# Kernel optimization log

Measured on AMD Instinct MI355X. Metric: run time of the kernel, lower is better.

## Reference

```python
import jax, jax.numpy as jnp
import numpy as np

N_NODES = 100000


def setup_inputs() -> dict:
    key = jax.random.key(0)
    ks = jax.random.split(key, 4)
    x = jax.random.normal(ks[0], (N_NODES, 128), dtype=jnp.float32)
    edge_index = jax.random.randint(ks[1], (2, 1600000), 0, N_NODES, dtype=jnp.int64)
    W1 = jax.random.normal(ks[2], (128, 64), dtype=jnp.float32) * (1.0 / np.sqrt(128))
    b1 = jnp.zeros((64,), dtype=jnp.float32)
    W2 = jax.random.normal(ks[3], (64, 64), dtype=jnp.float32) * (1.0 / np.sqrt(64))
    b2 = jnp.zeros((64,), dtype=jnp.float32)
    return {"x": x, "edge_index": edge_index, "W1": W1, "b1": b1, "W2": W2, "b2": b2}


def reference(x, edge_index, W1, b1, W2, b2):
    N = x.shape[0]
    loop = jnp.arange(N, dtype=edge_index.dtype)
    src = jnp.concatenate([edge_index[0], loop])  # [E+N] sources (incl. self-loops)
    dst = jnp.concatenate([edge_index[1], loop])  # [E+N] targets
    # symmetric GCN normalization: deg counts edge weights (all 1) at target nodes
    deg = jax.ops.segment_sum(jnp.ones_like(src, dtype=x.dtype), dst, num_segments=N)
    dinv = jnp.where(deg > 0, jax.lax.rsqrt(deg), 0.0)
    norm = (dinv[src] * dinv[dst])[:, None]  # [E+N, 1]

    def gcn_conv(h, W, b):
        h = h @ W                                   # dense transform [N, out]
        msg = h[src] * norm                         # gather + normalize [E+N, out]
        agg = jax.ops.segment_sum(msg, dst, num_segments=N)  # scatter-add
        return agg + b

    h = jax.nn.gelu(gcn_conv(x, W1, b1), approximate=False)  # torch nn.GELU = exact erf
    return gcn_conv(h, W2, b2)
```

## Files before the change

kernel.cpp:

```cpp
#include <hip/hip_runtime.h>
#include <math.h>

#define N_NODES 100000
#define N_EDGES 1600000
#define NBUK 782
#define BCAP 2600
#define BINCHUNK 4096

typedef unsigned short u16;
typedef u16 u16x4 __attribute__((ext_vector_type(4)));
typedef u16 u16x8 __attribute__((ext_vector_type(8)));
typedef short s16x8 __attribute__((ext_vector_type(8)));
typedef float f32x4 __attribute__((ext_vector_type(4)));

__device__ __forceinline__ float bf2f(u16 u) {
    union { unsigned i; float f; } v; v.i = ((unsigned)u) << 16; return v.f;
}
__device__ __forceinline__ u16 f2bf(float f) {
    union { float f; unsigned i; } v; v.f = f;
    return (u16)((v.i + 0x7FFFu + ((v.i >> 16) & 1u)) >> 16);
}

__global__ __launch_bounds__(256) void k_bin(const int* __restrict__ src,
                                             const int* __restrict__ dst,
                                             int* bucketCursor,
                                             unsigned int* __restrict__ bins) {
    __shared__ int lcnt[NBUK];
    __shared__ int lbase[NBUK];
    const int t = threadIdx.x;
    for (int i = t; i < NBUK; i += 256) lcnt[i] = 0;
    __syncthreads();

    const int e0 = blockIdx.x * BINCHUNK + t * 16;
    int4 s4[4], d4[4];
    int bkt[16], rnk[16];
    const bool valid = e0 < N_EDGES;
    if (valid) {
        #pragma unroll
        for (int k = 0; k < 4; ++k) {
            s4[k] = *(const int4*)(src + e0 + 4 * k);
            d4[k] = *(const int4*)(dst + e0 + 4 * k);
        }
        #pragma unroll
        for (int k = 0; k < 4; ++k) {
            int dd[4] = { d4[k].x, d4[k].y, d4[k].z, d4[k].w };
            #pragma unroll
            for (int j = 0; j < 4; ++j) {
                int b = dd[j] >> 7;
                bkt[4 * k + j] = b;
                rnk[4 * k + j] = atomicAdd(&lcnt[b], 1);
            }
        }
    }
    __syncthreads();
    for (int i = t; i < NBUK; i += 256)
        if (lcnt[i] > 0) lbase[i] = atomicAdd(&bucketCursor[i], lcnt[i]);
    __syncthreads();
    if (valid) {
        #pragma unroll
        for (int k = 0; k < 4; ++k) {
            int ss[4] = { s4[k].x, s4[k].y, s4[k].z, s4[k].w };
            int dd[4] = { d4[k].x, d4[k].y, d4[k].z, d4[k].w };
            #pragma unroll
            for (int j = 0; j < 4; ++j) {
                int i = 4 * k + j;
                unsigned w = ((unsigned)(dd[j] & 127) << 17) | (unsigned)ss[j];
                bins[(size_t)bkt[i] * BCAP + lbase[bkt[i]] + rnk[i]] = w;
            }
        }
    }
}

__global__ __launch_bounds__(256) void k_bscan(const int* __restrict__ bucketCursor,
                                               int* __restrict__ gBase,
                                               int* __restrict__ row_start) {
    __shared__ int sd[256];
    const int t = threadIdx.x;
    const int idx0 = t * 4;
    int v0 = (idx0 + 0 < NBUK) ? bucketCursor[idx0 + 0] : 0;
    int v1 = (idx0 + 1 < NBUK) ? bucketCursor[idx0 + 1] : 0;
    int v2 = (idx0 + 2 < NBUK) ? bucketCursor[idx0 + 2] : 0;
    int v3 = (idx0 + 3 < NBUK) ? bucketCursor[idx0 + 3] : 0;
    int s0 = v0, s1 = s0 + v1, s2 = s1 + v2, s3 = s2 + v3;
    sd[t] = s3;
    __syncthreads();
    #pragma unroll
    for (int off = 1; off < 256; off <<= 1) {
        int x = (t >= off) ? sd[t - off] : 0;
        __syncthreads();
        sd[t] += x;
        __syncthreads();
    }
    int excl = (t > 0) ? sd[t - 1] : 0;
    if (idx0 + 0 < NBUK) gBase[idx0 + 0] = excl;
    if (idx0 + 1 < NBUK) gBase[idx0 + 1] = excl + s0;
    if (idx0 + 2 < NBUK) gBase[idx0 + 2] = excl + s1;
    if (idx0 + 3 < NBUK) gBase[idx0 + 3] = excl + s2;
    if (t == 0) row_start[N_NODES] = N_EDGES;
}

__global__ __launch_bounds__(256) void k_build(const unsigned int* __restrict__ bins,
                                               const int* __restrict__ bucketCursor,
                                               const int* __restrict__ gBase,
                                               int* __restrict__ row_start,
                                               float* __restrict__ dinv,
                                               int* __restrict__ csr_src) {
    __shared__ int cnt[128];
    __shared__ int ps[128];
    __shared__ int cur[128];
    const int b = blockIdx.x;
    const int t = threadIdx.x;
    const int bcnt = bucketCursor[b];
    const int gb = gBase[b];
    const unsigned int* mybins = bins + (size_t)b * BCAP;

    if (t < 128) cnt[t] = 0;
    __syncthreads();
    for (int i = t; i < bcnt; i += 256)
        atomicAdd(&cnt[mybins[i] >> 17], 1);
    __syncthreads();
    if (t < 128) ps[t] = cnt[t];
    __syncthreads();
    #pragma unroll
    for (int off = 1; off < 128; off <<= 1) {
        int x = (t >= off && t < 128) ? ps[t - off] : 0;
        __syncthreads();
        if (t < 128) ps[t] += x;
        __syncthreads();
    }
    if (t < 128) {
        int excl = (t > 0) ? ps[t - 1] : 0;
        cur[t] = excl;
        int node = (b << 7) + t;
        if (node < N_NODES) {
            row_start[node] = gb + excl;
            dinv[node] = rsqrtf((float)(cnt[t] + 1));
        }
    }
    __syncthreads();
    for (int i = t; i < bcnt; i += 256) {
        unsigned w = mybins[i];
        int dl = w >> 17;
        int s = (int)(w & 0x1FFFFu);
        int p = atomicAdd(&cur[dl], 1);
        csr_src[gb + p] = s;
    }
}

__global__ __launch_bounds__(256) void k_wsplit(const float* __restrict__ W1,
                                                const float* __restrict__ W2,
                                                u16* __restrict__ w1pre,
                                                u16* __restrict__ w2pre) {
    const int t = threadIdx.x;
    #pragma unroll
    for (int i = 0; i < 32; ++i) {
        int e = i * 256 + t;
        int k = e >> 6, c = e & 63;
        float f = W1[e];
        u16 h = f2bf(f);
        u16 l = f2bf(f - bf2f(h));
        int byte = (c * 256 + k * 2) ^ ((c & 7) << 4);
        *(u16*)((char*)w1pre + byte) = h;
        *(u16*)((char*)w1pre + 16384 + byte) = l;
    }
    #pragma unroll
    for (int i = 0; i < 16; ++i) {
        int e = i * 256 + t;
        int k = e >> 6, c = e & 63;
        float f = W2[e];
        u16 h = f2bf(f);
        u16 l = f2bf(f - bf2f(h));
        int byte = (c * 128 + k * 2) ^ ((c & 7) << 4);
        *(u16*)((char*)w2pre + byte) = h;
        *(u16*)((char*)w2pre + 8192 + byte) = l;
    }
}

__global__ __launch_bounds__(256) void k_gemm1(const float* __restrict__ X,
                                               const u16* __restrict__ w1pre,
                                               const float* __restrict__ dinv,
                                               u16* __restrict__ H) {
    __shared__ u16 sxh[64 * 128];
    __shared__ u16 sxl[64 * 128];
    __shared__ u16 wth[64 * 128];
    __shared__ u16 wtl[64 * 128];
    const int t = threadIdx.x;
    const int blk = blockIdx.x;

    {
        const float4* Xv = (const float4*)X;
        #pragma unroll
        for (int i = 0; i < 8; ++i) {
            int idx = i * 256 + t;
            int row = idx >> 5;
            int k4  = (idx & 31) << 2;
            int grow = blk * 64 + row;
            float4 v = make_float4(0.f, 0.f, 0.f, 0.f);
            if (grow < N_NODES) v = Xv[(size_t)grow * 32 + (idx & 31)];
            float f[4] = { v.x, v.y, v.z, v.w };
            u16x4 hv, lv;
            #pragma unroll
            for (int j = 0; j < 4; ++j) {
                u16 h = f2bf(f[j]);
                hv[j] = h;
                lv[j] = f2bf(f[j] - bf2f(h));
            }
            int byte = (row * 256 + k4 * 2) ^ ((row & 7) << 4);
            *(u16x4*)((char*)sxh + byte) = hv;
            *(u16x4*)((char*)sxl + byte) = lv;
        }
    }
    {
        const u16x8* G = (const u16x8*)w1pre;
        u16x8* Lh = (u16x8*)wth;
        u16x8* Ll = (u16x8*)wtl;
        #pragma unroll
        for (int i = 0; i < 4; ++i) Lh[i * 256 + t] = G[i * 256 + t];
        #pragma unroll
        for (int i = 0; i < 4; ++i) Ll[i * 256 + t] = G[1024 + i * 256 + t];
    }
    __syncthreads();

    const int lane = t & 63;
    const int w    = t >> 6;
    const int l16  = lane & 15;
    const int kg   = lane >> 4;
    f32x4 acc[4];
    #pragma unroll
    for (int nt = 0; nt < 4; ++nt)
        #pragma unroll
        for (int j = 0; j < 4; ++j) acc[nt][j] = 0.f;

    const int arow = w * 16 + l16;
    const int aswz = (arow & 7) << 4;
    #pragma unroll
    for (int kt = 0; kt < 4; ++kt) {
        const int koff = kt * 64 + kg * 16;
        s16x8 ah = *(const s16x8*)((const char*)sxh + ((arow * 256 + koff) ^ aswz));
        s16x8 al = *(const s16x8*)((const char*)sxl + ((arow * 256 + koff) ^ aswz));
        #pragma unroll
        for (int nt = 0; nt < 4; ++nt) {
            const int c = nt * 16 + l16;
            const int wb = (c * 256 + koff) ^ ((c & 7) << 4);
            s16x8 bh = *(const s16x8*)((const char*)wth + wb);
            s16x8 bl = *(const s16x8*)((const char*)wtl + wb);
            acc[nt] = __builtin_amdgcn_mfma_f32_16x16x32_bf16(ah, bh, acc[nt], 0, 0, 0);
            acc[nt] = __builtin_amdgcn_mfma_f32_16x16x32_bf16(ah, bl, acc[nt], 0, 0, 0);
            acc[nt] = __builtin_amdgcn_mfma_f32_16x16x32_bf16(al, bh, acc[nt], 0, 0, 0);
        }
    }
    const int rbase = blk * 64 + w * 16 + kg * 4;
    #pragma unroll
    for (int reg = 0; reg < 4; ++reg) {
        int row = rbase + reg;
        float di = (row < N_NODES) ? dinv[row] : 0.f;
        #pragma unroll
        for (int nt = 0; nt < 4; ++nt)
            __builtin_nontemporal_store(f2bf(acc[nt][reg] * di),
                                        &H[(size_t)row * 64 + nt * 16 + l16]);
    }
}

__global__ __launch_bounds__(256) void k_gemm2(const u16* __restrict__ Xb,
                                               const u16* __restrict__ w2pre,
                                               const float* __restrict__ dinv,
                                               u16* __restrict__ H) {
    __shared__ u16 sxb[64 * 64];
    __shared__ u16 wth[64 * 64];
    __shared__ u16 wtl[64 * 64];
    const int t = threadIdx.x;
    const int blk = blockIdx.x;

    {
        const u16x8* Xv = (const u16x8*)Xb;
        #pragma unroll
        for (int i = 0; i < 2; ++i) {
            int idx = i * 256 + t;
            int row = idx >> 3;
            int k0  = (idx & 7) << 3;
            int grow = blk * 64 + row;
            u16x8 v;
            #pragma unroll
            for (int j = 0; j < 8; ++j) v[j] = 0;
            if (grow < N_NODES) v = Xv[(size_t)grow * 8 + (idx & 7)];
            int byte = (row * 128 + k0 * 2) ^ ((row & 7) << 4);
            *(u16x8*)((char*)sxb + byte) = v;
        }
    }
    {
        const u16x8* G = (const u16x8*)w2pre;
        u16x8* Lh = (u16x8*)wth;
        u16x8* Ll = (u16x8*)wtl;
        #pragma unroll
        for (int i = 0; i < 2; ++i) Lh[i * 256 + t] = G[i * 256 + t];
        #pragma unroll
        for (int i = 0; i < 2; ++i) Ll[i * 256 + t] = G[512 + i * 256 + t];
    }
    __syncthreads();

    const int lane = t & 63;
    const int w    = t >> 6;
    const int l16  = lane & 15;
    const int kg   = lane >> 4;
    f32x4 acc[4];
    #pragma unroll
    for (int nt = 0; nt < 4; ++nt)
        #pragma unroll
        for (int j = 0; j < 4; ++j) acc[nt][j] = 0.f;

    const int arow = w * 16 + l16;
    const int aswz = (arow & 7) << 4;
    #pragma unroll
    for (int kt = 0; kt < 2; ++kt) {
        const int koff = kt * 64 + kg * 16;
        s16x8 a = *(const s16x8*)((const char*)sxb + ((arow * 128 + koff) ^ aswz));
        #pragma unroll
        for (int nt = 0; nt < 4; ++nt) {
            const int c = nt * 16 + l16;
            const int wb = (c * 128 + koff) ^ ((c & 7) << 4);
            s16x8 bh = *(const s16x8*)((const char*)wth + wb);
            s16x8 bl = *(const s16x8*)((const char*)wtl + wb);
            acc[nt] = __builtin_amdgcn_mfma_f32_16x16x32_bf16(a, bh, acc[nt], 0, 0, 0);
            acc[nt] = __builtin_amdgcn_mfma_f32_16x16x32_bf16(a, bl, acc[nt], 0, 0, 0);
        }
    }
    const int rbase = blk * 64 + w * 16 + kg * 4;
    #pragma unroll
    for (int reg = 0; reg < 4; ++reg) {
        int row = rbase + reg;
        float di = (row < N_NODES) ? dinv[row] : 0.f;
        #pragma unroll
        for (int nt = 0; nt < 4; ++nt)
            __builtin_nontemporal_store(f2bf(acc[nt][reg] * di),
                                        &H[(size_t)row * 64 + nt * 16 + l16]);
    }
}

template <bool GELU>
__global__ __launch_bounds__(256) void k_aggregate(const u16* __restrict__ hs,
                                                   const int* __restrict__ csr_src,
                                                   const int* __restrict__ row_start,
                                                   const float* __restrict__ dinv,
                                                   const float* __restrict__ b,
                                                   void* __restrict__ outraw) {
    const int t = threadIdx.x;
    const int lane = t & 63;
    const int node = __builtin_amdgcn_readfirstlane(blockIdx.x * 4 + (t >> 6));
    const int jS = __builtin_amdgcn_readfirstlane(row_start[node]);
    const int jE = __builtin_amdgcn_readfirstlane(row_start[node + 1]);
    const int deg = jE - jS;
    const u16* __restrict__ colp = hs + lane;

    int raw[32];
    #pragma unroll
    for (int i = 0; i < 32; ++i)
        raw[i] = __builtin_amdgcn_readfirstlane(csr_src[jS + i]);

    float acc = bf2f(colp[(size_t)node << 6]);
    u16 v[32];
    #pragma unroll
    for (int i = 0; i < 32; ++i) {
        int idx = (i < deg) ? raw[i] : N_NODES;
        v[i] = colp[(size_t)(unsigned)idx << 6];
    }
    #pragma unroll
    for (int i = 0; i < 32; ++i) acc += bf2f(v[i]);

    if (deg > 32) {
        for (int j = jS + 32; j < jE; ++j) {
            int idx = __builtin_amdgcn_readfirstlane(csr_src[j]);
            acc += bf2f(colp[(size_t)(unsigned)idx << 6]);
        }
    }

    float r = dinv[node] * acc + b[lane];
    if (GELU) {
        r = 0.5f * r * (1.0f + erff(r * 0.70710678118654752f));
        ((u16*)outraw)[((size_t)node << 6) + lane] = f2bf(r);
    } else {
        ((float*)outraw)[((size_t)node << 6) + lane] = r;
    }
}

extern "C" void kernel_launch(void* const* d_in, const int* in_sizes, int n_in,
                              void* d_out, int out_size, void* d_ws, size_t ws_size,
                              hipStream_t stream) {
    const float* x  = (const float*)d_in[0];
    const int* edge = (const int*)d_in[1];
    const float* W1 = (const float*)d_in[2];
    const float* b1 = (const float*)d_in[3];
    const float* W2 = (const float*)d_in[4];
    const float* b2 = (const float*)d_in[5];
    float* out = (float*)d_out;

    const int* src = edge;
    const int* dst = edge + N_EDGES;

    char* ws = (char*)d_ws;
    int*   bucketCursor = (int*)(ws);
    int*   gBase        = (int*)(ws + 4096);
    int*   row_start    = (int*)(ws + 8192);
    float* dinv         = (float*)(ws + 408576);
    int*   csr_src      = (int*)(ws + 808960);
    u16*   hsb          = (u16*)(ws + 7209088);
    unsigned int* bins  = (unsigned int*)hsb;
    u16*   out1b        = (u16*)(ws + 20013184);
    u16*   w1pre        = (u16*)(ws + 32817280);
    u16*   w2pre        = (u16*)(ws + 32850048);

    const int nBlkBin  = (N_EDGES + BINCHUNK - 1) / BINCHUNK;
    const int nBlkGemm = (N_NODES + 63) / 64;
    const int nBlkAgg  = N_NODES / 4;

    hipMemsetAsync(bucketCursor, 0, NBUK * sizeof(int), stream);
    k_wsplit<<<1, 256, 0, stream>>>(W1, W2, w1pre, w2pre);
    k_bin<<<nBlkBin, 256, 0, stream>>>(src, dst, bucketCursor, bins);
    k_bscan<<<1, 256, 0, stream>>>(bucketCursor, gBase, row_start);
    k_build<<<NBUK, 256, 0, stream>>>(bins, bucketCursor, gBase, row_start, dinv, csr_src);

    k_gemm1<<<nBlkGemm, 256, 0, stream>>>(x, w1pre, dinv, hsb);
    k_aggregate<true><<<nBlkAgg, 256, 0, stream>>>(hsb, csr_src, row_start, dinv, b1, out1b);

    k_gemm2<<<nBlkGemm, 256, 0, stream>>>(out1b, w2pre, dinv, hsb);
    k_aggregate<false><<<nBlkAgg, 256, 0, stream>>>(hsb, csr_src, row_start, dinv, b2, out);
}
```

Before: 177.4 us.

## Quantize transformed node features to int8 with per-row scales for aggregation

The GEMM epilogues now quantize each output row to int8 with a per-row absmax scale instead of storing bf16, and the aggregation kernels gather int8 values and multiply by the source row's scale. This halves the bytes moved by the random neighbor gathers, which dominate the aggregation cost, at the price of an extra scale load per edge and a larger quantization error. The weight-splitting kernel is also spread over 32 blocks instead of one, and the GEMM grid is padded to a multiple of 64 rows so the padding row N_NODES gets valid zero data and scale.

```diff
diff --git a/kernel.cpp b/kernel.cpp
--- a/kernel.cpp
+++ b/kernel.cpp
@@ -3,6 +3,7 @@
 
 #define N_NODES 100000
 #define N_EDGES 1600000
+#define NROWS 100032
 #define NBUK 782
 #define BCAP 2600
 #define BINCHUNK 4096
@@ -152,20 +153,21 @@
                                                 u16* __restrict__ w1pre,
                                                 u16* __restrict__ w2pre) {
     const int t = threadIdx.x;
-    #pragma unroll
-    for (int i = 0; i < 32; ++i) {
-        int e = i * 256 + t;
-        int k = e >> 6, c = e & 63;
-        float f = W1[e];
-        u16 h = f2bf(f);
-        u16 l = f2bf(f - bf2f(h));
-        int byte = (c * 256 + k * 2) ^ ((c & 7) << 4);
-        *(u16*)((char*)w1pre + byte) = h;
-        *(u16*)((char*)w1pre + 16384 + byte) = l;
-    }
-    #pragma unroll
-    for (int i = 0; i < 16; ++i) {
-        int e = i * 256 + t;
+    const int b = blockIdx.x;
+    if (b < 16) {
+        #pragma unroll
+        for (int half = 0; half < 2; ++half) {
+            int e = b * 512 + half * 256 + t;
+            int k = e >> 6, c = e & 63;
+            float f = W1[e];
+            u16 h = f2bf(f);
+            u16 l = f2bf(f - bf2f(h));
+            int byte = (c * 256 + k * 2) ^ ((c & 7) << 4);
+            *(u16*)((char*)w1pre + byte) = h;
+            *(u16*)((char*)w1pre + 16384 + byte) = l;
+        }
+    } else {
+        int e = (b - 16) * 256 + t;
         int k = e >> 6, c = e & 63;
         float f = W2[e];
         u16 h = f2bf(f);
@@ -176,10 +178,29 @@
     }
 }
 
+__device__ __forceinline__ void quant_store_row(float v0, float v1, float v2, float v3,
+                                                int row, int l16,
+                                                signed char* __restrict__ H8,
+                                                float* __restrict__ scale) {
+    float m = fmaxf(fmaxf(fabsf(v0), fabsf(v1)), fmaxf(fabsf(v2), fabsf(v3)));
+    m = fmaxf(m, __shfl_xor(m, 1));
+    m = fmaxf(m, __shfl_xor(m, 2));
+    m = fmaxf(m, __shfl_xor(m, 4));
+    m = fmaxf(m, __shfl_xor(m, 8));
+    float inv = (m > 0.f) ? 127.f / m : 0.f;
+    if (l16 == 0) scale[row] = m * (1.f / 127.f);
+    size_t base = (size_t)row * 64 + l16;
+    H8[base +  0] = (signed char)__float2int_rn(v0 * inv);
+    H8[base + 16] = (signed char)__float2int_rn(v1 * inv);
+    H8[base + 32] = (signed char)__float2int_rn(v2 * inv);
+    H8[base + 48] = (signed char)__float2int_rn(v3 * inv);
+}
+
 __global__ __launch_bounds__(256) void k_gemm1(const float* __restrict__ X,
                                                const u16* __restrict__ w1pre,
                                                const float* __restrict__ dinv,
-                                               u16* __restrict__ H) {
+                                               signed char* __restrict__ H8,
+                                               float* __restrict__ scale) {
     __shared__ u16 sxh[64 * 128];
     __shared__ u16 sxl[64 * 128];
     __shared__ u16 wth[64 * 128];
@@ -254,17 +275,17 @@
     for (int reg = 0; reg < 4; ++reg) {
         int row = rbase + reg;
         float di = (row < N_NODES) ? dinv[row] : 0.f;
-        #pragma unroll
-        for (int nt = 0; nt < 4; ++nt)
-            __builtin_nontemporal_store(f2bf(acc[nt][reg] * di),
-                                        &H[(size_t)row * 64 + nt * 16 + l16]);
+        quant_store_row(acc[0][reg] * di, acc[1][reg] * di,
+                        acc[2][reg] * di, acc[3][reg] * di,
+                        row, l16, H8, scale);
     }
 }
 
 __global__ __launch_bounds__(256) void k_gemm2(const u16* __restrict__ Xb,
                                                const u16* __restrict__ w2pre,
                                                const float* __restrict__ dinv,
-                                               u16* __restrict__ H) {
+                                               signed char* __restrict__ H8,
+                                               float* __restrict__ scale) {
     __shared__ u16 sxb[64 * 64];
     __shared__ u16 wth[64 * 64];
     __shared__ u16 wtl[64 * 64];
@@ -329,15 +350,15 @@
     for (int reg = 0; reg < 4; ++reg) {
         int row = rbase + reg;
         float di = (row < N_NODES) ? dinv[row] : 0.f;
-        #pragma unroll
-        for (int nt = 0; nt < 4; ++nt)
-            __builtin_nontemporal_store(f2bf(acc[nt][reg] * di),
-                                        &H[(size_t)row * 64 + nt * 16 + l16]);
+        quant_store_row(acc[0][reg] * di, acc[1][reg] * di,
+                        acc[2][reg] * di, acc[3][reg] * di,
+                        row, l16, H8, scale);
     }
 }
 
 template <bool GELU>
-__global__ __launch_bounds__(256) void k_aggregate(const u16* __restrict__ hs,
+__global__ __launch_bounds__(256) void k_aggregate(const signed char* __restrict__ hs8,
+                                                   const float* __restrict__ scale,
                                                    const int* __restrict__ csr_src,
                                                    const int* __restrict__ row_start,
                                                    const float* __restrict__ dinv,
@@ -349,27 +370,28 @@
     const int jS = __builtin_amdgcn_readfirstlane(row_start[node]);
     const int jE = __builtin_amdgcn_readfirstlane(row_start[node + 1]);
     const int deg = jE - jS;
-    const u16* __restrict__ colp = hs + lane;
-
-    int raw[32];
+    const signed char* __restrict__ colp = hs8 + lane;
+
+    int idx[32];
+    #pragma unroll
+    for (int i = 0; i < 32; ++i) {
+        int r = __builtin_amdgcn_readfirstlane(csr_src[jS + i]);
+        idx[i] = (i < deg) ? r : N_NODES;
+    }
+
+    float acc = (float)colp[(size_t)node << 6] * scale[node];
+    signed char v[32];
     #pragma unroll
     for (int i = 0; i < 32; ++i)
-        raw[i] = __builtin_amdgcn_readfirstlane(csr_src[jS + i]);
-
-    float acc = bf2f(colp[(size_t)node << 6]);
-    u16 v[32];
-    #pragma unroll
-    for (int i = 0; i < 32; ++i) {
-        int idx = (i < deg) ? raw[i] : N_NODES;
-        v[i] = colp[(size_t)(unsigned)idx << 6];
-    }
-    #pragma unroll
-    for (int i = 0; i < 32; ++i) acc += bf2f(v[i]);
+        v[i] = colp[(size_t)(unsigned)idx[i] << 6];
+    #pragma unroll
+    for (int i = 0; i < 32; ++i)
+        acc += (float)v[i] * scale[idx[i]];
 
     if (deg > 32) {
         for (int j = jS + 32; j < jE; ++j) {
-            int idx = __builtin_amdgcn_readfirstlane(csr_src[j]);
-            acc += bf2f(colp[(size_t)(unsigned)idx << 6]);
+            int r = __builtin_amdgcn_readfirstlane(csr_src[j]);
+            acc += (float)colp[(size_t)(unsigned)r << 6] * scale[r];
         }
     }
 
@@ -402,25 +424,28 @@
     int*   row_start    = (int*)(ws + 8192);
     float* dinv         = (float*)(ws + 408576);
     int*   csr_src      = (int*)(ws + 808960);
-    u16*   hsb          = (u16*)(ws + 7209088);
-    unsigned int* bins  = (unsigned int*)hsb;
-    u16*   out1b        = (u16*)(ws + 20013184);
-    u16*   w1pre        = (u16*)(ws + 32817280);
-    u16*   w2pre        = (u16*)(ws + 32850048);
+    float* scale1       = (float*)(ws + 7209216);
+    float* scale2       = (float*)(ws + 7609344);
+    signed char* hs8a   = (signed char*)(ws + 8009472);
+    signed char* hs8b   = (signed char*)(ws + 14411520);
+    u16*   out1b        = (u16*)(ws + 20813568);
+    unsigned int* bins  = (unsigned int*)out1b;
+    u16*   w1pre        = (u16*)(ws + 33617664);
+    u16*   w2pre        = (u16*)(ws + 33650432);
 
     const int nBlkBin  = (N_EDGES + BINCHUNK - 1) / BINCHUNK;
-    const int nBlkGemm = (N_NODES + 63) / 64;
+    const int nBlkGemm = NROWS / 64;
     const int nBlkAgg  = N_NODES / 4;
 
     hipMemsetAsync(bucketCursor, 0, NBUK * sizeof(int), stream);
-    k_wsplit<<<1, 256, 0, stream>>>(W1, W2, w1pre, w2pre);
+    k_wsplit<<<32, 256, 0, stream>>>(W1, W2, w1pre, w2pre);
     k_bin<<<nBlkBin, 256, 0, stream>>>(src, dst, bucketCursor, bins);
     k_bscan<<<1, 256, 0, stream>>>(bucketCursor, gBase, row_start);
     k_build<<<NBUK, 256, 0, stream>>>(bins, bucketCursor, gBase, row_start, dinv, csr_src);
 
-    k_gemm1<<<nBlkGemm, 256, 0, stream>>>(x, w1pre, dinv, hsb);
-    k_aggregate<true><<<nBlkAgg, 256, 0, stream>>>(hsb, csr_src, row_start, dinv, b1, out1b);
-
-    k_gemm2<<<nBlkGemm, 256, 0, stream>>>(out1b, w2pre, dinv, hsb);
-    k_aggregate<false><<<nBlkAgg, 256, 0, stream>>>(hsb, csr_src, row_start, dinv, b2, out);
-}
+    k_gemm1<<<nBlkGemm, 256, 0, stream>>>(x, w1pre, dinv, hs8a, scale1);
+    k_aggregate<true><<<nBlkAgg, 256, 0, stream>>>(hs8a, scale1, csr_src, row_start, dinv, b1, out1b);
+
+    k_gemm2<<<nBlkGemm, 256, 0, stream>>>(out1b, w2pre, dinv, hs8b, scale2);
+    k_aggregate<false><<<nBlkAgg, 256, 0, stream>>>(hs8b, scale2, csr_src, row_start, dinv, b2, out);
+}
```

Result: slower. 237.5 us (+33.9%).

## Split aggregation across column halves and even/odd edges, parallelize weight split

Applied to the files above, without the earlier changes.

The aggregate kernel now launches two blocks per node group. Each block handles 32 of the 64 feature columns, and the two half-waves take even and odd neighbors respectively, with results combined by a cross-lane shuffle. This doubles wave count and halves the serial gather chain per lane, aiming to raise memory-level parallelism for the bf16 gathers. The cost is more redundant index loads and half-width (32x2B) row segments per gather. The weight split kernel is also spread over 32 blocks, and workspace offsets and GEMM grid are adjusted to the padded row count. Tail edges beyond 32 are processed only by the low half-wave, while the high half reads the zero-row sentinel.

```diff
diff --git a/kernel.cpp b/kernel.cpp
--- a/kernel.cpp
+++ b/kernel.cpp
@@ -3,6 +3,7 @@
 
 #define N_NODES 100000
 #define N_EDGES 1600000
+#define NROWS 100032
 #define NBUK 782
 #define BCAP 2600
 #define BINCHUNK 4096
@@ -152,20 +153,21 @@
                                                 u16* __restrict__ w1pre,
                                                 u16* __restrict__ w2pre) {
     const int t = threadIdx.x;
-    #pragma unroll
-    for (int i = 0; i < 32; ++i) {
-        int e = i * 256 + t;
-        int k = e >> 6, c = e & 63;
-        float f = W1[e];
-        u16 h = f2bf(f);
-        u16 l = f2bf(f - bf2f(h));
-        int byte = (c * 256 + k * 2) ^ ((c & 7) << 4);
-        *(u16*)((char*)w1pre + byte) = h;
-        *(u16*)((char*)w1pre + 16384 + byte) = l;
-    }
-    #pragma unroll
-    for (int i = 0; i < 16; ++i) {
-        int e = i * 256 + t;
+    const int b = blockIdx.x;
+    if (b < 16) {
+        #pragma unroll
+        for (int half = 0; half < 2; ++half) {
+            int e = b * 512 + half * 256 + t;
+            int k = e >> 6, c = e & 63;
+            float f = W1[e];
+            u16 h = f2bf(f);
+            u16 l = f2bf(f - bf2f(h));
+            int byte = (c * 256 + k * 2) ^ ((c & 7) << 4);
+            *(u16*)((char*)w1pre + byte) = h;
+            *(u16*)((char*)w1pre + 16384 + byte) = l;
+        }
+    } else {
+        int e = (b - 16) * 256 + t;
         int k = e >> 6, c = e & 63;
         float f = W2[e];
         u16 h = f2bf(f);
@@ -344,41 +346,54 @@
                                                    const float* __restrict__ b,
                                                    void* __restrict__ outraw) {
     const int t = threadIdx.x;
+    const int half = blockIdx.x & 1;
+    const int grp  = blockIdx.x >> 1;
     const int lane = t & 63;
-    const int node = __builtin_amdgcn_readfirstlane(blockIdx.x * 4 + (t >> 6));
+    const int col  = (half << 5) | (lane & 31);
+    const bool hi  = lane >= 32;
+    const int node = __builtin_amdgcn_readfirstlane(grp * 4 + (t >> 6));
     const int jS = __builtin_amdgcn_readfirstlane(row_start[node]);
     const int jE = __builtin_amdgcn_readfirstlane(row_start[node + 1]);
     const int deg = jE - jS;
-    const u16* __restrict__ colp = hs + lane;
+    const u16* __restrict__ colp = hs + col;
 
     int raw[32];
     #pragma unroll
     for (int i = 0; i < 32; ++i)
         raw[i] = __builtin_amdgcn_readfirstlane(csr_src[jS + i]);
 
-    float acc = bf2f(colp[(size_t)node << 6]);
-    u16 v[32];
-    #pragma unroll
-    for (int i = 0; i < 32; ++i) {
-        int idx = (i < deg) ? raw[i] : N_NODES;
-        v[i] = colp[(size_t)(unsigned)idx << 6];
-    }
-    #pragma unroll
-    for (int i = 0; i < 32; ++i) acc += bf2f(v[i]);
+    int selfIdx = hi ? N_NODES : node;
+    float acc = bf2f(colp[(size_t)(unsigned)selfIdx << 6]);
+
+    u16 v[16];
+    #pragma unroll
+    for (int i = 0; i < 16; ++i) {
+        int ea = (2 * i     < deg) ? raw[2 * i]     : N_NODES;
+        int eb = (2 * i + 1 < deg) ? raw[2 * i + 1] : N_NODES;
+        int r = hi ? eb : ea;
+        v[i] = colp[(size_t)(unsigned)r << 6];
+    }
+    #pragma unroll
+    for (int i = 0; i < 16; ++i) acc += bf2f(v[i]);
 
     if (deg > 32) {
         for (int j = jS + 32; j < jE; ++j) {
-            int idx = __builtin_amdgcn_readfirstlane(csr_src[j]);
-            acc += bf2f(colp[(size_t)(unsigned)idx << 6]);
-        }
-    }
-
-    float r = dinv[node] * acc + b[lane];
-    if (GELU) {
-        r = 0.5f * r * (1.0f + erff(r * 0.70710678118654752f));
-        ((u16*)outraw)[((size_t)node << 6) + lane] = f2bf(r);
-    } else {
-        ((float*)outraw)[((size_t)node << 6) + lane] = r;
+            int r0 = __builtin_amdgcn_readfirstlane(csr_src[j]);
+            int r = hi ? N_NODES : r0;
+            acc += bf2f(colp[(size_t)(unsigned)r << 6]);
+        }
+    }
+
+    acc += __shfl_xor(acc, 32);
+
+    if (!hi) {
+        float r = dinv[node] * acc + b[col];
+        if (GELU) {
+            r = 0.5f * r * (1.0f + erff(r * 0.70710678118654752f));
+            ((u16*)outraw)[((size_t)node << 6) + col] = f2bf(r);
+        } else {
+            ((float*)outraw)[((size_t)node << 6) + col] = r;
+        }
     }
 }
 
@@ -402,25 +417,25 @@
     int*   row_start    = (int*)(ws + 8192);
     float* dinv         = (float*)(ws + 408576);
     int*   csr_src      = (int*)(ws + 808960);
-    u16*   hsb          = (u16*)(ws + 7209088);
+    u16*   hsb          = (u16*)(ws + 7209216);
     unsigned int* bins  = (unsigned int*)hsb;
-    u16*   out1b        = (u16*)(ws + 20013184);
-    u16*   w1pre        = (u16*)(ws + 32817280);
-    u16*   w2pre        = (u16*)(ws + 32850048);
+    u16*   out1b        = (u16*)(ws + 20013312);
+    u16*   w1pre        = (u16*)(ws + 32817408);
+    u16*   w2pre        = (u16*)(ws + 32850176);
 
     const int nBlkBin  = (N_EDGES + BINCHUNK - 1) / BINCHUNK;
-    const int nBlkGemm = (N_NODES + 63) / 64;
-    const int nBlkAgg  = N_NODES / 4;
+    const int nBlkGemm = NROWS / 64;
+    const int nBlkAggH = (N_NODES / 4) * 2;
 
     hipMemsetAsync(bucketCursor, 0, NBUK * sizeof(int), stream);
-    k_wsplit<<<1, 256, 0, stream>>>(W1, W2, w1pre, w2pre);
+    k_wsplit<<<32, 256, 0, stream>>>(W1, W2, w1pre, w2pre);
     k_bin<<<nBlkBin, 256, 0, stream>>>(src, dst, bucketCursor, bins);
     k_bscan<<<1, 256, 0, stream>>>(bucketCursor, gBase, row_start);
     k_build<<<NBUK, 256, 0, stream>>>(bins, bucketCursor, gBase, row_start, dinv, csr_src);
 
     k_gemm1<<<nBlkGemm, 256, 0, stream>>>(x, w1pre, dinv, hsb);
-    k_aggregate<true><<<nBlkAgg, 256, 0, stream>>>(hsb, csr_src, row_start, dinv, b1, out1b);
+    k_aggregate<true><<<nBlkAggH, 256, 0, stream>>>(hsb, csr_src, row_start, dinv, b1, out1b);
 
     k_gemm2<<<nBlkGemm, 256, 0, stream>>>(out1b, w2pre, dinv, hsb);
-    k_aggregate<false><<<nBlkAgg, 256, 0, stream>>>(hsb, csr_src, row_start, dinv, b2, out);
-}
+    k_aggregate<false><<<nBlkAggH, 256, 0, stream>>>(hsb, csr_src, row_start, dinv, b2, out);
+}
```

After: 207.4 us. 16.9% more time.
